# Optimization experiments

Measured on AMD Instinct MI355X. Metric: run time of the kernel, lower is better.

Reference implementation:

```python
import jax, jax.numpy as jnp
import numpy as np

SOFTENING = 1e-6
EPS = 1e-9
CUTOFF = 0.1
K_NEG = 4
MARGIN = 1.0
KE_FACTOR = 1e-3


def setup_inputs() -> dict:
    key = jax.random.key(0)
    ks = jax.random.split(key, 16)
    B, S, D8, W = 4, 2048, 8, 16
    N = B * S
    return {
        "positions_2d": jax.random.normal(ks[0], (B, S, 2), dtype=jnp.float32),
        "masses": jax.random.uniform(ks[1], (B, S, 1), dtype=jnp.float32),
        "vel_2d": jax.random.normal(ks[2], (N, 2), dtype=jnp.float32),
        "pos_8d": jax.random.normal(ks[3], (N, D8), dtype=jnp.float32),
        "pos_pos_2d": jax.random.normal(ks[4], (N, 2), dtype=jnp.float32),
        "pos_pos_8d": jax.random.normal(ks[5], (N, D8), dtype=jnp.float32),
        "positive_masses": jax.random.uniform(ks[6], (N, 1), dtype=jnp.float32),
        "neg_pos_2d": jax.random.normal(ks[7], (N * K_NEG, 2), dtype=jnp.float32),
        "neg_pos_8d": jax.random.normal(ks[8], (N * K_NEG, D8), dtype=jnp.float32),
        "neg_masses": jax.random.uniform(ks[9], (N * K_NEG, 1), dtype=jnp.float32),
        "exp_masses": jax.random.uniform(ks[10], (N * K_NEG, 1), dtype=jnp.float32),
        "G": jnp.float32(1.0),
        "repulsion_strength": jnp.float32(0.5),
        "well_centers": jax.random.normal(ks[11], (W, D8), dtype=jnp.float32),
        "well_strength": jnp.float32(0.1),
        "temperature": jnp.float32(1.0),
        "entropy_coeff": jnp.float32(0.01),
    }


def _calculate_forces(positions_2d, masses, G, repulsion_strength):
    # positions_2d: [B,S,2], masses: [B,S,1]
    B, S, _ = positions_2d.shape
    # diff[b,i,j] = pos[b,j] - pos[b,i]  -> [B,S,S,2]
    diff = positions_2d[:, None, :, :] - positions_2d[:, :, None, :]
    dist_sq = jnp.sum(diff * diff, axis=-1) + SOFTENING  # [B,S,S]
    dist = jnp.sqrt(dist_sq)
    diag = jnp.eye(S, dtype=bool)  # [S,S], broadcasts over B
    dist_safe = jnp.where(diag, 1.0, dist)
    dist_sq_safe = jnp.where(diag, 1.0, dist_sq)
    mm = masses[:, :, None, 0] * masses[:, None, :, 0]  # [B,S,S]
    attractive = jax.nn.relu(G) * mm / dist_sq_safe
    rep_strength = jax.nn.relu(repulsion_strength)
    repulsive = rep_strength * jax.nn.relu(1.0 - dist_safe / CUTOFF) / (dist_sq_safe * dist_safe + EPS)
    total_mag = repulsive - attractive  # [B,S,S]
    force_vectors = total_mag[..., None] * diff / (dist_safe[..., None] + EPS)
    return jnp.sum(force_vectors, axis=2)  # [B,S,2]


def _cdist(a, b):
    # Euclidean cdist: [N,D] x [W,D] -> [N,W]; W=16 so dense is cheap
    d = a[:, None, :] - b[None, :, :]
    return jnp.sqrt(jnp.sum(d * d, axis=-1))


def _grand_unifying_loss(pos_2d, vel_2d, pos_8d, masses_flat, pos_pos_2d, pos_pos_8d,
                         positive_masses, neg_pos_2d, neg_pos_8d, neg_masses, exp_masses,
                         G, well_centers, well_strength, temperature, entropy_coeff):
    Gp = jax.nn.relu(G)
    dist_pos_2d = jnp.linalg.norm(pos_2d - pos_pos_2d, axis=-1) + EPS  # [N]
    pe_pairwise_pos = -Gp * (masses_flat * positive_masses)[:, 0] / dist_pos_2d
    pos_2d_rep = jnp.repeat(pos_2d, K_NEG, axis=0)  # [N*K,2]
    dist_neg_2d = jnp.linalg.norm(pos_2d_rep - neg_pos_2d, axis=-1) + EPS
    pe_pairwise_neg = -Gp * (exp_masses * neg_masses)[:, 0] / dist_neg_2d

    ws = jax.nn.relu(well_strength)
    all_pos_8d = jnp.concatenate([pos_8d, pos_pos_8d], axis=0)  # [2N,8]
    min_dist_pos = jnp.min(_cdist(all_pos_8d, well_centers), axis=1)
    pe_well_pos = ws * min_dist_pos ** 2
    all_neg_8d = jnp.concatenate([jnp.repeat(pos_8d, K_NEG, axis=0), neg_pos_8d], axis=0)
    min_dist_neg = jnp.min(_cdist(all_neg_8d, well_centers), axis=1)
    pe_well_neg = ws * min_dist_neg ** 2

    U_pos = jnp.mean(pe_pairwise_pos) + jnp.mean(pe_well_pos)
    U_neg = jnp.mean(pe_pairwise_neg) + jnp.mean(pe_well_neg)
    batch_variance = jnp.mean(jnp.var(all_pos_8d, axis=0, ddof=1))  # torch.var is unbiased
    entropy_term = jax.nn.relu(temperature) * jax.nn.relu(entropy_coeff) * batch_variance
    F_pos = U_pos - entropy_term
    F_neg = U_neg - entropy_term
    free_energy_loss = jax.nn.relu(MARGIN + F_pos - F_neg)
    # Original: mean(masses[N,1] * ke[N]) broadcasts to an [N,N] outer product;
    # mean of the outer product == mean(m) * mean(ke) (same value and gradients)
    ke = jnp.sum(vel_2d * vel_2d, axis=-1)  # [N]
    ke_loss = KE_FACTOR * 0.5 * jnp.mean(masses_flat) * jnp.mean(ke)
    return free_energy_loss + ke_loss


def reference(positions_2d, masses, vel_2d, pos_8d, pos_pos_2d, pos_pos_8d,
              positive_masses, neg_pos_2d, neg_pos_8d, neg_masses, exp_masses,
              G, repulsion_strength, well_centers, well_strength, temperature, entropy_coeff):
    forces = _calculate_forces(positions_2d, masses, G, repulsion_strength)
    pos_flat = positions_2d.reshape(-1, 2)
    masses_flat = masses.reshape(-1, 1)
    loss = _grand_unifying_loss(pos_flat, vel_2d, pos_8d, masses_flat, pos_pos_2d,
                                pos_pos_8d, positive_masses, neg_pos_2d, neg_pos_8d,
                                neg_masses, exp_masses, G, well_centers, well_strength,
                                temperature, entropy_coeff)
    return forces, loss
```

## Files before the change

### kernel.cpp

```cpp
#include <hip/hip_runtime.h>

#define SEQ    2048
#define N_PTS  8192
#define NK     32768
#define N2     16384
#define NACC   22
#define NLOSSBLK 256
#define NFORCE   1024
#define SLOT_DOUBLES (NLOSSBLK * NACC)
#define CTR_OFFSET   (SLOT_DOUBLES * 8)

__device__ __forceinline__ float frcp(float x)  { return __builtin_amdgcn_rcpf(x); }
__device__ __forceinline__ float fsqrt_(float x){ return __builtin_amdgcn_sqrtf(x); }

__device__ __forceinline__ float min_dist2(float4 a, float4 b, const float* __restrict__ wc)
{
    float best = 3.4e38f;
    #pragma unroll
    for (int w = 0; w < 16; ++w) {
        const float* c = &wc[w * 8];
        float d, s;
        d = a.x - c[0]; s = d * d;
        d = a.y - c[1]; s = fmaf(d, d, s);
        d = a.z - c[2]; s = fmaf(d, d, s);
        d = a.w - c[3]; s = fmaf(d, d, s);
        d = b.x - c[4]; s = fmaf(d, d, s);
        d = b.y - c[5]; s = fmaf(d, d, s);
        d = b.z - c[6]; s = fmaf(d, d, s);
        d = b.w - c[7]; s = fmaf(d, d, s);
        best = fminf(best, s);
    }
    return best;
}

__global__ __launch_bounds__(256, 4) void fused_kernel(
    const float* __restrict__ pos,
    const float* __restrict__ mass,
    const float* __restrict__ vel,
    const float* __restrict__ pos8,
    const float* __restrict__ pp2,
    const float* __restrict__ pp8,
    const float* __restrict__ pmass,
    const float* __restrict__ negp2,
    const float* __restrict__ negp8,
    const float* __restrict__ negm,
    const float* __restrict__ expm,
    const float* __restrict__ Gptr,
    const float* __restrict__ Rptr,
    const float* __restrict__ wellc,
    const float* __restrict__ wstr,
    const float* __restrict__ tPtr,
    const float* __restrict__ ecPtr,
    float* __restrict__ out,
    double* __restrict__ slots,
    unsigned int* __restrict__ ctr)
{
    const int tid = threadIdx.x;
    const int blk = blockIdx.x;

    if (blk >= NLOSSBLK) {
        __shared__ float4 s4[SEQ];
        __shared__ float  rf[2][4][8];

        const int fb = blk - NLOSSBLK;
        const int b  = fb >> 8;
        const int it = fb & 255;
        const int rowbase = b * SEQ;

        const float2* p2 = (const float2*)pos;
        for (int k = tid; k < SEQ; k += 256) {
            const float2 v = p2[rowbase + k];
            s4[k] = make_float4(v.x, v.y, mass[rowbase + k], 0.0f);
        }
        const float Gv = fmaxf(Gptr[0], 0.0f);
        const float Rv = fmaxf(Rptr[0], 0.0f);
        __syncthreads();

        const int il = tid & 7;
        const int js = tid >> 3;
        const int iloc = it * 8 + il;
        const float px = s4[iloc].x;
        const float py = s4[iloc].y;
        const float ci = Gv * s4[iloc].z;

        auto pair = [&](const float4 q, float& fx, float& fy) {
            const float dx = q.x - px;
            const float dy = q.y - py;
            const float r2 = fmaf(dx, dx, fmaf(dy, dy, 1e-6f));
            const float r  = fsqrt_(r2);
            const float rp = r + 1e-9f;
            float mor = -(ci * q.z) * frcp(r2 * rp);
            const float t = fmaf(-10.0f, r, 1.0f);
            if (t > 0.0f) {
                mor += (Rv * t) * frcp(fmaf(r2, r, 1e-9f) * rp);
            }
            fx = fmaf(mor, dx, fx);
            fy = fmaf(mor, dy, fy);
        };

        float fx0 = 0.0f, fy0 = 0.0f, fx1 = 0.0f, fy1 = 0.0f;
        float fx2 = 0.0f, fy2 = 0.0f, fx3 = 0.0f, fy3 = 0.0f;
        const int j0 = js * 64;
        #pragma unroll 2
        for (int jj = 0; jj < 64; jj += 4) {
            const float4 q0 = s4[j0 + jj + 0];
            const float4 q1 = s4[j0 + jj + 1];
            const float4 q2 = s4[j0 + jj + 2];
            const float4 q3 = s4[j0 + jj + 3];
            pair(q0, fx0, fy0);
            pair(q1, fx1, fy1);
            pair(q2, fx2, fy2);
            pair(q3, fx3, fy3);
        }
        float vx = (fx0 + fx1) + (fx2 + fx3);
        float vy = (fy0 + fy1) + (fy2 + fy3);

        #pragma unroll
        for (int off = 32; off >= 8; off >>= 1) {
            vx += __shfl_down(vx, off, 64);
            vy += __shfl_down(vy, off, 64);
        }
        const int lane = tid & 63, wid = tid >> 6;
        if (lane < 8) { rf[0][wid][lane] = vx; rf[1][wid][lane] = vy; }
        __syncthreads();
        if (tid < 16) {
            const int comp = tid >> 3, i2 = tid & 7;
            const float s = (rf[comp][0][i2] + rf[comp][1][i2])
                          + (rf[comp][2][i2] + rf[comp][3][i2]);
            out[(rowbase + it * 8 + i2) * 2 + comp] = s;
        }
        return;
    }

    __shared__ float  wc[128];
    __shared__ double red[4][NACC];
    __shared__ int    lastflag;

    if (tid < 128) wc[tid] = wellc[tid];
    if (tid == 0)  lastflag = 0;
    __syncthreads();

    const int lb  = blk;
    const int idx = lb * 256 + tid;

    double acc[NACC];
    #pragma unroll
    for (int k = 0; k < NACC; ++k) acc[k] = 0.0;

    {
        const float* row = (idx < NK) ? (pos8 + (idx >> 2) * 8)
                                      : (negp8 + (idx - NK) * 8);
        const float4 a = ((const float4*)row)[0];
        const float4 b = ((const float4*)row)[1];
        acc[3] = (double)min_dist2(a, b, wc);
    }
    if (idx < NK) {
        const int i = idx >> 2;
        const float dx = pos[i * 2 + 0] - negp2[idx * 2 + 0];
        const float dy = pos[i * 2 + 1] - negp2[idx * 2 + 1];
        const float d  = fsqrt_(fmaf(dx, dx, dy * dy)) + 1e-9f;
        acc[1] = (double)(expm[idx] * negm[idx] / d);
    }
    if (idx < N2) {
        const float* row = (idx < N_PTS) ? (pos8 + idx * 8)
                                         : (pp8 + (idx - N_PTS) * 8);
        const float4 a = ((const float4*)row)[0];
        const float4 b = ((const float4*)row)[1];
        acc[2] = (double)min_dist2(a, b, wc);
        acc[4]  = (double)a.x;  acc[12] = (double)(a.x * a.x);
        acc[5]  = (double)a.y;  acc[13] = (double)(a.y * a.y);
        acc[6]  = (double)a.z;  acc[14] = (double)(a.z * a.z);
        acc[7]  = (double)a.w;  acc[15] = (double)(a.w * a.w);
        acc[8]  = (double)b.x;  acc[16] = (double)(b.x * b.x);
        acc[9]  = (double)b.y;  acc[17] = (double)(b.y * b.y);
        acc[10] = (double)b.z;  acc[18] = (double)(b.z * b.z);
        acc[11] = (double)b.w;  acc[19] = (double)(b.w * b.w);
    }
    if (idx < N_PTS) {
        const float dx = pos[idx * 2 + 0] - pp2[idx * 2 + 0];
        const float dy = pos[idx * 2 + 1] - pp2[idx * 2 + 1];
        const float d  = fsqrt_(fmaf(dx, dx, dy * dy)) + 1e-9f;
        acc[0]  = (double)(mass[idx] * pmass[idx] / d);
        acc[20] = (double)mass[idx];
        const float vx = vel[idx * 2 + 0];
        const float vy = vel[idx * 2 + 1];
        acc[21] = (double)fmaf(vx, vx, vy * vy);
    }

    const int lane = tid & 63, wid = tid >> 6;
    #pragma unroll
    for (int k = 0; k < NACC; ++k) {
        double v = acc[k];
        for (int off = 32; off > 0; off >>= 1) v += __shfl_down(v, off, 64);
        if (lane == 0) red[wid][k] = v;
    }
    __syncthreads();
    if (tid < NACC) {
        slots[lb * NACC + tid] = red[0][tid] + red[1][tid] + red[2][tid] + red[3][tid];
    }
    __syncthreads();
    if (tid == 0) {
        __threadfence();
        const unsigned int ticket = atomicAdd(ctr, 1u);
        if (ticket == (NLOSSBLK - 1u) ||
            ticket == 0xAAAAAAAAu + (NLOSSBLK - 1u)) lastflag = 1;
    }
    __syncthreads();
    if (!lastflag) return;

    __threadfence();
    #pragma unroll
    for (int k = 0; k < NACC; ++k) {
        double v = slots[tid * NACC + k];
        for (int off = 32; off > 0; off >>= 1) v += __shfl_down(v, off, 64);
        if (lane == 0) red[wid][k] = v;
    }
    __syncthreads();
    if (tid == 0) {
        double s[NACC];
        #pragma unroll
        for (int k = 0; k < NACC; ++k)
            s[k] = red[0][k] + red[1][k] + red[2][k] + red[3][k];

        const double Gp  = fmax((double)Gptr[0], 0.0);
        const double wsp = fmax((double)wstr[0], 0.0);
        const double T   = fmax((double)tPtr[0], 0.0);
        const double ec  = fmax((double)ecPtr[0], 0.0);
        const double Nd = 8192.0, NKd = 32768.0, N2d = 16384.0, NK2d = 65536.0;

        const double U_pos = -Gp * s[0] / Nd  + wsp * s[2] / N2d;
        const double U_neg = -Gp * s[1] / NKd + wsp * s[3] / NK2d;

        double var = 0.0;
        for (int d = 0; d < 8; ++d) {
            const double sx_ = s[4 + d], sxx = s[12 + d];
            var += (sxx - sx_ * sx_ / N2d) / (N2d - 1.0);
        }
        var *= 0.125;
        const double ent = T * ec * var;
        const double Fp = U_pos - ent, Fn = U_neg - ent;
        double fel = 1.0 + Fp - Fn;
        if (fel < 0.0) fel = 0.0;
        const double ke_loss = 1e-3 * 0.5 * (s[20] / Nd) * (s[21] / Nd);
        out[16384] = (float)(fel + ke_loss);
    }
}

extern "C" void kernel_launch(void* const* d_in, const int* in_sizes, int n_in,
                              void* d_out, int out_size, void* d_ws, size_t ws_size,
                              hipStream_t stream)
{
    const float* pos   = (const float*)d_in[0];
    const float* mass  = (const float*)d_in[1];
    const float* vel   = (const float*)d_in[2];
    const float* pos8  = (const float*)d_in[3];
    const float* pp2   = (const float*)d_in[4];
    const float* pp8   = (const float*)d_in[5];
    const float* pmass = (const float*)d_in[6];
    const float* negp2 = (const float*)d_in[7];
    const float* negp8 = (const float*)d_in[8];
    const float* negm  = (const float*)d_in[9];
    const float* expm  = (const float*)d_in[10];
    const float* Gp    = (const float*)d_in[11];
    const float* Rp    = (const float*)d_in[12];
    const float* wellc = (const float*)d_in[13];
    const float* wstr  = (const float*)d_in[14];
    const float* temp  = (const float*)d_in[15];
    const float* ecoef = (const float*)d_in[16];

    float*        out   = (float*)d_out;
    double*       slots = (double*)d_ws;
    unsigned int* ctr   = (unsigned int*)((char*)d_ws + CTR_OFFSET);

    fused_kernel<<<NLOSSBLK + NFORCE, 256, 0, stream>>>(pos, mass, vel, pos8, pp2,
                                          pp8, pmass, negp2, negp8, negm, expm,
                                          Gp, Rp, wellc, wstr, temp, ecoef,
                                          out, slots, ctr);
}
```

Measured before the change: 119.9 us.

## Split fused kernel into separate loss and force kernels with strided j access

Splits the single fused launch into a loss kernel and a force kernel, so each is compiled with its own register budget and the force path no longer carries the loss path's double-precision accumulator pressure. The force loop now reads shared memory with a stride of 32 across threads instead of contiguous 64-element chunks, which changes the LDS bank access pattern. The unroll factor also goes from 2 to 4. The two kernels now run back to back on the same stream instead of concurrently in one grid, which adds a launch and may give up overlap between loss and force work.

New measurement: 118.7 us. About the same (-1.0%).

```diff
diff --git a/kernel.cpp b/kernel.cpp
--- a/kernel.cpp
+++ b/kernel.cpp
@@ -33,7 +33,87 @@
     return best;
 }
 
-__global__ __launch_bounds__(256, 4) void fused_kernel(
+
+__global__ __launch_bounds__(256, 4) void force_kernel(
+    const float* __restrict__ pos,
+    const float* __restrict__ mass,
+    const float* __restrict__ Gptr,
+    const float* __restrict__ Rptr,
+    float* __restrict__ out)
+{
+    __shared__ float4 s4[SEQ];
+    __shared__ float  rf[2][4][8];
+
+    const int tid = threadIdx.x;
+    const int fb  = blockIdx.x;
+    const int b   = fb >> 8;
+    const int it  = fb & 255;
+    const int rowbase = b * SEQ;
+
+    const float2* p2 = (const float2*)pos;
+    for (int k = tid; k < SEQ; k += 256) {
+        const float2 v = p2[rowbase + k];
+        s4[k] = make_float4(v.x, v.y, mass[rowbase + k], 0.0f);
+    }
+    const float Gv = fmaxf(Gptr[0], 0.0f);
+    const float Rv = fmaxf(Rptr[0], 0.0f);
+    __syncthreads();
+
+    const int il = tid & 7;
+    const int js = tid >> 3;
+    const int iloc = it * 8 + il;
+    const float px = s4[iloc].x;
+    const float py = s4[iloc].y;
+    const float ci = Gv * s4[iloc].z;
+
+    auto pair = [&](const float4 q, float& fx, float& fy) {
+        const float dx = q.x - px;
+        const float dy = q.y - py;
+        const float r2 = fmaf(dx, dx, fmaf(dy, dy, 1e-6f));
+        const float r  = fsqrt_(r2);
+        const float rp = r + 1e-9f;
+        float mor = -(ci * q.z) * frcp(r2 * rp);
+        const float t = fmaf(-10.0f, r, 1.0f);
+        if (t > 0.0f) {
+            mor += (Rv * t) * frcp(fmaf(r2, r, 1e-9f) * rp);
+        }
+        fx = fmaf(mor, dx, fx);
+        fy = fmaf(mor, dy, fy);
+    };
+
+    float fx0 = 0.0f, fy0 = 0.0f, fx1 = 0.0f, fy1 = 0.0f;
+    float fx2 = 0.0f, fy2 = 0.0f, fx3 = 0.0f, fy3 = 0.0f;
+    #pragma unroll 4
+    for (int kk = 0; kk < 64; kk += 4) {
+        const float4 q0 = s4[js + 32 * (kk + 0)];
+        const float4 q1 = s4[js + 32 * (kk + 1)];
+        const float4 q2 = s4[js + 32 * (kk + 2)];
+        const float4 q3 = s4[js + 32 * (kk + 3)];
+        pair(q0, fx0, fy0);
+        pair(q1, fx1, fy1);
+        pair(q2, fx2, fy2);
+        pair(q3, fx3, fy3);
+    }
+    float vx = (fx0 + fx1) + (fx2 + fx3);
+    float vy = (fy0 + fy1) + (fy2 + fy3);
+
+    #pragma unroll
+    for (int off = 32; off >= 8; off >>= 1) {
+        vx += __shfl_down(vx, off, 64);
+        vy += __shfl_down(vy, off, 64);
+    }
+    const int lane = tid & 63, wid = tid >> 6;
+    if (lane < 8) { rf[0][wid][lane] = vx; rf[1][wid][lane] = vy; }
+    __syncthreads();
+    if (tid < 16) {
+        const int comp = tid >> 3, i2 = tid & 7;
+        const float s = (rf[comp][0][i2] + rf[comp][1][i2])
+                      + (rf[comp][2][i2] + rf[comp][3][i2]);
+        out[(rowbase + it * 8 + i2) * 2 + comp] = s;
+    }
+}
+
+__global__ __launch_bounds__(256) void loss_kernel(
     const float* __restrict__ pos,
     const float* __restrict__ mass,
     const float* __restrict__ vel,
@@ -46,7 +126,6 @@
     const float* __restrict__ negm,
     const float* __restrict__ expm,
     const float* __restrict__ Gptr,
-    const float* __restrict__ Rptr,
     const float* __restrict__ wellc,
     const float* __restrict__ wstr,
     const float* __restrict__ tPtr,
@@ -57,80 +136,6 @@
 {
     const int tid = threadIdx.x;
     const int blk = blockIdx.x;
-
-    if (blk >= NLOSSBLK) {
-        __shared__ float4 s4[SEQ];
-        __shared__ float  rf[2][4][8];
-
-        const int fb = blk - NLOSSBLK;
-        const int b  = fb >> 8;
-        const int it = fb & 255;
-        const int rowbase = b * SEQ;
-
-        const float2* p2 = (const float2*)pos;
-        for (int k = tid; k < SEQ; k += 256) {
-            const float2 v = p2[rowbase + k];
-            s4[k] = make_float4(v.x, v.y, mass[rowbase + k], 0.0f);
-        }
-        const float Gv = fmaxf(Gptr[0], 0.0f);
-        const float Rv = fmaxf(Rptr[0], 0.0f);
-        __syncthreads();
-
-        const int il = tid & 7;
-        const int js = tid >> 3;
-        const int iloc = it * 8 + il;
-        const float px = s4[iloc].x;
-        const float py = s4[iloc].y;
-        const float ci = Gv * s4[iloc].z;
-
-        auto pair = [&](const float4 q, float& fx, float& fy) {
-            const float dx = q.x - px;
-            const float dy = q.y - py;
-            const float r2 = fmaf(dx, dx, fmaf(dy, dy, 1e-6f));
-            const float r  = fsqrt_(r2);
-            const float rp = r + 1e-9f;
-            float mor = -(ci * q.z) * frcp(r2 * rp);
-            const float t = fmaf(-10.0f, r, 1.0f);
-            if (t > 0.0f) {
-                mor += (Rv * t) * frcp(fmaf(r2, r, 1e-9f) * rp);
-            }
-            fx = fmaf(mor, dx, fx);
-            fy = fmaf(mor, dy, fy);
-        };
-
-        float fx0 = 0.0f, fy0 = 0.0f, fx1 = 0.0f, fy1 = 0.0f;
-        float fx2 = 0.0f, fy2 = 0.0f, fx3 = 0.0f, fy3 = 0.0f;
-        const int j0 = js * 64;
-        #pragma unroll 2
-        for (int jj = 0; jj < 64; jj += 4) {
-            const float4 q0 = s4[j0 + jj + 0];
-            const float4 q1 = s4[j0 + jj + 1];
-            const float4 q2 = s4[j0 + jj + 2];
-            const float4 q3 = s4[j0 + jj + 3];
-            pair(q0, fx0, fy0);
-            pair(q1, fx1, fy1);
-            pair(q2, fx2, fy2);
-            pair(q3, fx3, fy3);
-        }
-        float vx = (fx0 + fx1) + (fx2 + fx3);
-        float vy = (fy0 + fy1) + (fy2 + fy3);
-
-        #pragma unroll
-        for (int off = 32; off >= 8; off >>= 1) {
-            vx += __shfl_down(vx, off, 64);
-            vy += __shfl_down(vy, off, 64);
-        }
-        const int lane = tid & 63, wid = tid >> 6;
-        if (lane < 8) { rf[0][wid][lane] = vx; rf[1][wid][lane] = vy; }
-        __syncthreads();
-        if (tid < 16) {
-            const int comp = tid >> 3, i2 = tid & 7;
-            const float s = (rf[comp][0][i2] + rf[comp][1][i2])
-                          + (rf[comp][2][i2] + rf[comp][3][i2]);
-            out[(rowbase + it * 8 + i2) * 2 + comp] = s;
-        }
-        return;
-    }
 
     __shared__ float  wc[128];
     __shared__ double red[4][NACC];
@@ -272,8 +277,9 @@
     double*       slots = (double*)d_ws;
     unsigned int* ctr   = (unsigned int*)((char*)d_ws + CTR_OFFSET);
 
-    fused_kernel<<<NLOSSBLK + NFORCE, 256, 0, stream>>>(pos, mass, vel, pos8, pp2,
-                                          pp8, pmass, negp2, negp8, negm, expm,
-                                          Gp, Rp, wellc, wstr, temp, ecoef,
-                                          out, slots, ctr);
-}
+    loss_kernel<<<NLOSSBLK, 256, 0, stream>>>(pos, mass, vel, pos8, pp2, pp8,
+                                              pmass, negp2, negp8, negm, expm,
+                                              Gp, wellc, wstr, temp, ecoef,
+                                              out, slots, ctr);
+    force_kernel<<<NFORCE, 256, 0, stream>>>(pos, mass, Gp, Rp, out);
+}
```
